# Kernel tuning notes

Measured on AMD Instinct MI355X. Metric: run time of the kernel, lower is better.

## Reference

```python
import jax, jax.numpy as jnp
import numpy as np

D_MODEL = 256
N_HEAD = 8


def setup_inputs() -> dict:
    key = jax.random.key(0)
    ks = jax.random.split(key, 9)
    B, S, D = 2, 2048, D_MODEL
    s = 1.0 / np.sqrt(D)
    return {
        "x": jax.random.normal(ks[0], (B, S, D), dtype=jnp.float32),
        "wq": jax.random.uniform(ks[1], (D, D), jnp.float32, -s, s),
        "bq": jax.random.uniform(ks[2], (D,), jnp.float32, -s, s),
        "wk": jax.random.uniform(ks[3], (D, D), jnp.float32, -s, s),
        "bk": jax.random.uniform(ks[4], (D,), jnp.float32, -s, s),
        "wv": jax.random.uniform(ks[5], (D, D), jnp.float32, -s, s),
        "bv": jax.random.uniform(ks[6], (D,), jnp.float32, -s, s),
        "wc": jax.random.uniform(ks[7], (D, D), jnp.float32, -s, s),
        "bc": jax.random.uniform(ks[8], (D,), jnp.float32, -s, s),
    }


def _split_heads(t):
    # [B, S, D] -> [B, H, S, D/H]
    B, S, D = t.shape
    return t.reshape(B, S, N_HEAD, D // N_HEAD).transpose(0, 2, 1, 3)


def reference(x, wq, bq, wk, bk, wv, bv, wc, bc):
    q = _split_heads(x @ wq.T + bq)
    k = _split_heads(x @ wk.T + bk)
    v = _split_heads(x @ wv.T + bv)
    d_head = q.shape[-1]
    # full [B, H, S, S] score matrix, as in the original (non-fused)
    score = jnp.einsum("bhqd,bhkd->bhqk", q, k) / jnp.sqrt(jnp.float32(d_head))
    attn = jax.nn.softmax(score, axis=-1)
    out = jnp.einsum("bhqk,bhkd->bhqd", attn, v)
    B, H, S, Dh = out.shape
    out = out.transpose(0, 2, 1, 3).reshape(B, S, H * Dh)
    out = out @ wc.T + bc
    attention = jnp.mean(attn, axis=1)  # [B, S, S]
    return (out, attention)
```

## Files before the change

kernel.cpp:

```cpp
#include <hip/hip_runtime.h>
#include <hip/hip_bf16.h>


#define B_   2
#define S_   2048
#define D_   256
#define H_   8
#define DH_  32
#define NROW (B_*S_)
#define KSPLIT 4
#define KKEYS (S_/KSPLIT)

typedef __attribute__((ext_vector_type(8))) short bf16x8;
typedef __attribute__((ext_vector_type(4))) float f32x4;

__device__ __forceinline__ f32x4 mfma_bf16(bf16x8 a, bf16x8 b, f32x4 c) {
    return __builtin_amdgcn_mfma_f32_16x16x32_bf16(a, b, c, 0, 0, 0);
}

__device__ __forceinline__ float fast_exp2(float x) {
    return __builtin_amdgcn_exp2f(x);
}

__device__ __forceinline__ unsigned short f2bf_bits(float v) {
    __hip_bfloat16 h = __float2bfloat16(v);
    return *reinterpret_cast<unsigned short*>(&h);
}

__device__ __forceinline__ size_t fragidx(int m, int k) {
    return (size_t)(m >> 4) * 4096 + (k >> 5) * 512 + ((k >> 3) & 3) * 128
           + (m & 15) * 8 + (k & 7);
}

__global__ void split_all(const float4* __restrict__ x,
                          const float4* __restrict__ wq, const float4* __restrict__ wk,
                          const float4* __restrict__ wv, const float4* __restrict__ wc,
                          ushort4* __restrict__ xh, ushort4* __restrict__ xl,
                          ushort4* __restrict__ wqh, ushort4* __restrict__ wql,
                          ushort4* __restrict__ wkh, ushort4* __restrict__ wkl,
                          ushort4* __restrict__ wvh, ushort4* __restrict__ wvl,
                          ushort4* __restrict__ wch, ushort4* __restrict__ wcl) {
    int i = blockIdx.x * 256 + threadIdx.x;
    const float4* src; ushort4 *ph, *pl; int off;
    if (i < 262144) { src = x; ph = xh; pl = xl; off = i; }
    else {
        int j = i - 262144;
        int rg = j >> 14; off = j & 16383;
        if (rg == 0)      { src = wq; ph = wqh; pl = wql; }
        else if (rg == 1) { src = wk; ph = wkh; pl = wkl; }
        else if (rg == 2) { src = wv; ph = wvh; pl = wvl; }
        else              { src = wc; ph = wch; pl = wcl; }
    }
    float4 v = src[off];
    float vv[4] = {v.x, v.y, v.z, v.w};
    ushort4 hb, lb;
    unsigned short* hp = (unsigned short*)&hb;
    unsigned short* lp = (unsigned short*)&lb;
    for (int c = 0; c < 4; c++) {
        __hip_bfloat16 h = __float2bfloat16(vv[c]);
        hp[c] = *reinterpret_cast<unsigned short*>(&h);
        lp[c] = f2bf_bits(vv[c] - __bfloat162float(h));
    }
    int m = off >> 6, k = (off & 63) * 4;
    size_t fi = fragidx(m, k);
    ph[fi >> 2] = hb;
    pl[fi >> 2] = lb;
}

__global__ __launch_bounds__(256) void qkv_gemm(
    const __hip_bfloat16* __restrict__ xh, const __hip_bfloat16* __restrict__ xl,
    const __hip_bfloat16* __restrict__ w0h, const __hip_bfloat16* __restrict__ w0l,
    const __hip_bfloat16* __restrict__ w1h, const __hip_bfloat16* __restrict__ w1l,
    const __hip_bfloat16* __restrict__ w2h, const __hip_bfloat16* __restrict__ w2l,
    const float* __restrict__ bq, const float* __restrict__ bk, const float* __restrict__ bvv,
    __hip_bfloat16* __restrict__ Qf, __hip_bfloat16* __restrict__ Kf,
    __hip_bfloat16* __restrict__ Vf)
{
    int z = blockIdx.z;
    const __hip_bfloat16* wh = (z==0) ? w0h : (z==1) ? w1h : w2h;
    const __hip_bfloat16* wl = (z==0) ? w0l : (z==1) ? w1l : w2l;
    const float* bias = (z==0) ? bq : (z==1) ? bk : bvv;
    const float sv = (z==0) ? 0.17677669529663687f * 1.4426950408889634f : 1.0f;

    int tid = threadIdx.x;
    int w = tid >> 6, lid = tid & 63, quad = lid >> 4, l15 = lid & 15;
    int row0 = blockIdx.x * 64 + (w >> 1) * 32;
    int col0 = blockIdx.y * 64 + (w & 1) * 32;

    f32x4 acc[2][2] = {};
#pragma unroll
    for (int k0 = 0; k0 < 256; k0 += 32) {
        bf16x8 ah[2], al[2], bh[2], bl[2];
        for (int mi = 0; mi < 2; mi++) {
            size_t ro = (size_t)((row0 + mi * 16) >> 4) * 4096 + (k0 >> 5) * 512 + lid * 8;
            ah[mi] = *(const bf16x8*)(xh + ro);
            al[mi] = *(const bf16x8*)(xl + ro);
        }
        for (int ni = 0; ni < 2; ni++) {
            size_t co = (size_t)((col0 + ni * 16) >> 4) * 4096 + (k0 >> 5) * 512 + lid * 8;
            bh[ni] = *(const bf16x8*)(wh + co);
            bl[ni] = *(const bf16x8*)(wl + co);
        }
        for (int mi = 0; mi < 2; mi++)
            for (int ni = 0; ni < 2; ni++) {
                acc[mi][ni] = mfma_bf16(ah[mi], bh[ni], acc[mi][ni]);
                acc[mi][ni] = mfma_bf16(ah[mi], bl[ni], acc[mi][ni]);
                acc[mi][ni] = mfma_bf16(al[mi], bh[ni], acc[mi][ni]);
            }
    }
    for (int mi = 0; mi < 2; mi++)
        for (int ni = 0; ni < 2; ni++) {
            int col = col0 + ni * 16 + l15;
            int h = col >> 5, dh = col & 31;
            float bvl = bias[col];
            for (int r = 0; r < 4; r++) {
                int row = row0 + mi * 16 + quad * 4 + r;
                int b = row >> 11, s = row & 2047;
                __hip_bfloat16 o = __float2bfloat16((acc[mi][ni][r] + bvl) * sv);
                size_t bh_base = (size_t)(b * H_ + h) * (S_ * DH_);
                if (z == 2) {
                    int oo = s & 31;
                    int slot = ((oo & 15) >> 2) * 8 + ((oo >> 4) << 2) + (oo & 3);
                    Vf[bh_base + (s >> 5) * 1024 + (dh >> 4) * 512
                       + (slot >> 3) * 128 + (dh & 15) * 8 + (slot & 7)] = o;
                } else {
                    size_t idx = bh_base + (s >> 4) * 512 + (dh >> 3) * 128
                                 + (s & 15) * 8 + (dh & 7);
                    if (z == 0) Qf[idx] = o; else Kf[idx] = o;
                }
            }
        }
}

__global__ __launch_bounds__(256) void attn_flash(
    const __hip_bfloat16* __restrict__ Qf, const __hip_bfloat16* __restrict__ Kf,
    const __hip_bfloat16* __restrict__ Vf,
    __hip_bfloat16* __restrict__ cth, __hip_bfloat16* __restrict__ ctl,
    float* __restrict__ invL)
{
    __shared__ float sO[KSPLIT][32][33];
    __shared__ float sL[KSPLIT][32];
    int f = blockIdx.x;
    int g = (f & 7) * 128 + (f >> 3);
    int qt = g & 63;
    int h = (g >> 6) & 7;
    int b = g >> 9;
    int q0 = qt * 32;
    int tid = threadIdx.x, w = tid >> 6, lid = tid & 63, quad = lid >> 4, l15 = lid & 15;
    size_t bh_base = (size_t)(b * H_ + h) * (S_ * DH_);
    const __hip_bfloat16* Qp = Qf + bh_base + (q0 >> 4) * 512 + lid * 8;
    const __hip_bfloat16* Kp = Kf + bh_base + lid * 8;
    const __hip_bfloat16* Vp = Vf + bh_base + lid * 8;
    bf16x8 qfA = *(const bf16x8*)Qp;
    bf16x8 qfB = *(const bf16x8*)(Qp + 512);
    f32x4 zacc = {};
    f32x4 oacc[2][2] = {};
    float lpA = 0.f, lpB = 0.f;

    int kbeg = w * KKEYS;
#pragma unroll 2
    for (int k0 = kbeg; k0 < kbeg + KKEYS; k0 += 32) {
        bf16x8 kf0 = *(const bf16x8*)(Kp + (k0 >> 4) * 512);
        bf16x8 kf1 = *(const bf16x8*)(Kp + (k0 >> 4) * 512 + 512);
        bf16x8 vf0 = *(const bf16x8*)(Vp + (k0 >> 5) * 1024);
        bf16x8 vf1 = *(const bf16x8*)(Vp + (k0 >> 5) * 1024 + 512);

        __builtin_amdgcn_s_setprio(1);
        f32x4 cA0 = mfma_bf16(kf0, qfA, zacc);
        f32x4 cA1 = mfma_bf16(kf1, qfA, zacc);
        f32x4 cB0 = mfma_bf16(kf0, qfB, zacc);
        f32x4 cB1 = mfma_bf16(kf1, qfB, zacc);
        __builtin_amdgcn_s_setprio(0);
        float eA0[4], eA1[4], eB0[4], eB1[4];
        for (int r = 0; r < 4; r++) {
            eA0[r] = fast_exp2(cA0[r]);
            eA1[r] = fast_exp2(cA1[r]);
            eB0[r] = fast_exp2(cB0[r]);
            eB1[r] = fast_exp2(cB1[r]);
        }
        lpA += eA0[0] + eA0[1] + eA0[2] + eA0[3] + eA1[0] + eA1[1] + eA1[2] + eA1[3];
        lpB += eB0[0] + eB0[1] + eB0[2] + eB0[3] + eB1[0] + eB1[1] + eB1[2] + eB1[3];
        union { bf16x8 v; __hip_bfloat162 h2[4]; } puA, puB;
        puA.h2[0] = __float22bfloat162_rn(make_float2(eA0[0], eA0[1]));
        puA.h2[1] = __float22bfloat162_rn(make_float2(eA0[2], eA0[3]));
        puA.h2[2] = __float22bfloat162_rn(make_float2(eA1[0], eA1[1]));
        puA.h2[3] = __float22bfloat162_rn(make_float2(eA1[2], eA1[3]));
        puB.h2[0] = __float22bfloat162_rn(make_float2(eB0[0], eB0[1]));
        puB.h2[1] = __float22bfloat162_rn(make_float2(eB0[2], eB0[3]));
        puB.h2[2] = __float22bfloat162_rn(make_float2(eB1[0], eB1[1]));
        puB.h2[3] = __float22bfloat162_rn(make_float2(eB1[2], eB1[3]));
        __builtin_amdgcn_s_setprio(1);
        oacc[0][0] = mfma_bf16(vf0, puA.v, oacc[0][0]);
        oacc[0][1] = mfma_bf16(vf1, puA.v, oacc[0][1]);
        oacc[1][0] = mfma_bf16(vf0, puB.v, oacc[1][0]);
        oacc[1][1] = mfma_bf16(vf1, puB.v, oacc[1][1]);
        __builtin_amdgcn_s_setprio(0);
    }
    lpA += __shfl_xor(lpA, 16);
    lpA += __shfl_xor(lpA, 32);
    lpB += __shfl_xor(lpB, 16);
    lpB += __shfl_xor(lpB, 32);

    for (int qg = 0; qg < 2; qg++)
        for (int dh2 = 0; dh2 < 2; dh2++)
            for (int r = 0; r < 4; r++)
                sO[w][qg * 16 + l15][dh2 * 16 + quad * 4 + r] = oacc[qg][dh2][r];
    if (lid < 16) { sL[w][lid] = lpA; sL[w][16 + lid] = lpB; }
    __syncthreads();

    int d = tid & 31, q = tid >> 5;
#pragma unroll
    for (int qq = q; qq < 32; qq += 8) {
        float l = sL[0][qq] + sL[1][qq] + sL[2][qq] + sL[3][qq];
        float o = sO[0][qq][d] + sO[1][qq][d] + sO[2][qq][d] + sO[3][qq][d];
        float inv = 1.0f / l;
        float val = o * inv;
        size_t fi = fragidx(b * S_ + q0 + qq, h * DH_ + d);
        __hip_bfloat16 hv = __float2bfloat16(val);
        cth[fi] = hv;
        ctl[fi] = __float2bfloat16(val - __bfloat162float(hv));
        if (d == 0) invL[(b * H_ + h) * S_ + q0 + qq] = inv;
    }
}

__global__ __launch_bounds__(256) void attn_out(
    const __hip_bfloat16* __restrict__ Qf, const __hip_bfloat16* __restrict__ Kf,
    const float* __restrict__ invL,
    const __hip_bfloat16* __restrict__ ch, const __hip_bfloat16* __restrict__ cl,
    const __hip_bfloat16* __restrict__ wh, const __hip_bfloat16* __restrict__ wl,
    const float* __restrict__ bias,
    float* __restrict__ attn, float* __restrict__ out)
{
    __shared__ float invbuf[H_ * 32];
    int bid = blockIdx.x;
    int tid = threadIdx.x, w = tid >> 6, lid = tid & 63, quad = lid >> 4, l15 = lid & 15;

    if (bid < 256) {
        int row0 = (bid & 63) * 64 + (w >> 1) * 32;
        int col0 = (bid >> 6) * 64 + (w & 1) * 32;

        f32x4 acc[2][2] = {};
#pragma unroll
        for (int k0 = 0; k0 < 256; k0 += 32) {
            bf16x8 ah[2], al[2], bh[2], bl[2];
            for (int mi = 0; mi < 2; mi++) {
                size_t ro = (size_t)((row0 + mi * 16) >> 4) * 4096 + (k0 >> 5) * 512 + lid * 8;
                ah[mi] = *(const bf16x8*)(ch + ro);
                al[mi] = *(const bf16x8*)(cl + ro);
            }
            for (int ni = 0; ni < 2; ni++) {
                size_t co = (size_t)((col0 + ni * 16) >> 4) * 4096 + (k0 >> 5) * 512 + lid * 8;
                bh[ni] = *(const bf16x8*)(wh + co);
                bl[ni] = *(const bf16x8*)(wl + co);
            }
            for (int mi = 0; mi < 2; mi++)
                for (int ni = 0; ni < 2; ni++) {
                    acc[mi][ni] = mfma_bf16(ah[mi], bh[ni], acc[mi][ni]);
                    acc[mi][ni] = mfma_bf16(ah[mi], bl[ni], acc[mi][ni]);
                    acc[mi][ni] = mfma_bf16(al[mi], bh[ni], acc[mi][ni]);
                }
        }
        for (int mi = 0; mi < 2; mi++)
            for (int ni = 0; ni < 2; ni++) {
                int col = col0 + ni * 16 + l15;
                float bvl = bias[col];
                for (int r = 0; r < 4; r++) {
                    int row = row0 + mi * 16 + quad * 4 + r;
                    out[(size_t)row * 256 + col] = acc[mi][ni][r] + bvl;
                }
            }
    } else {
        int f2 = bid - 256;
        int g = (f2 & 7) * 128 + (f2 >> 3);
        int qy = g & 63, kx = (g >> 6) & 7, b = g >> 9;
        int q0 = qy * 32;
        int k0 = kx * 256 + w * 64;
        invbuf[tid] = invL[(b * H_ + (tid >> 5)) * S_ + q0 + (tid & 31)] * 0.125f;
        __syncthreads();
        f32x4 zacc = {};
        float psum[2][4][4] = {};
        size_t bh0 = (size_t)b * H_ * (S_ * DH_);
        size_t qoff = (size_t)(q0 >> 4) * 512 + lid * 8;
        size_t koff = (size_t)(k0 >> 4) * 512 + lid * 8;

#pragma unroll 2
        for (int h = 0; h < H_; h++) {
            size_t nb = bh0 + (size_t)h * (S_ * DH_);
            bf16x8 qfA = *(const bf16x8*)(Qf + nb + qoff);
            bf16x8 qfB = *(const bf16x8*)(Qf + nb + qoff + 512);
            bf16x8 kf0 = *(const bf16x8*)(Kf + nb + koff);
            bf16x8 kf1 = *(const bf16x8*)(Kf + nb + koff + 512);
            bf16x8 kf2 = *(const bf16x8*)(Kf + nb + koff + 1024);
            bf16x8 kf3 = *(const bf16x8*)(Kf + nb + koff + 1536);

            float ilA[4], ilB[4];
            for (int r = 0; r < 4; r++) {
                ilA[r] = invbuf[h * 32 + quad * 4 + r];
                ilB[r] = invbuf[h * 32 + 16 + quad * 4 + r];
            }

            __builtin_amdgcn_s_setprio(1);
            f32x4 cA0 = mfma_bf16(qfA, kf0, zacc);
            f32x4 cA1 = mfma_bf16(qfA, kf1, zacc);
            f32x4 cA2 = mfma_bf16(qfA, kf2, zacc);
            f32x4 cA3 = mfma_bf16(qfA, kf3, zacc);
            f32x4 cB0 = mfma_bf16(qfB, kf0, zacc);
            f32x4 cB1 = mfma_bf16(qfB, kf1, zacc);
            f32x4 cB2 = mfma_bf16(qfB, kf2, zacc);
            f32x4 cB3 = mfma_bf16(qfB, kf3, zacc);
            __builtin_amdgcn_s_setprio(0);
            for (int r = 0; r < 4; r++) {
                psum[0][0][r] += fast_exp2(cA0[r]) * ilA[r];
                psum[0][1][r] += fast_exp2(cA1[r]) * ilA[r];
                psum[0][2][r] += fast_exp2(cA2[r]) * ilA[r];
                psum[0][3][r] += fast_exp2(cA3[r]) * ilA[r];
                psum[1][0][r] += fast_exp2(cB0[r]) * ilB[r];
                psum[1][1][r] += fast_exp2(cB1[r]) * ilB[r];
                psum[1][2][r] += fast_exp2(cB2[r]) * ilB[r];
                psum[1][3][r] += fast_exp2(cB3[r]) * ilB[r];
            }
        }
        for (int qg = 0; qg < 2; qg++)
            for (int nt = 0; nt < 4; nt++)
                for (int r = 0; r < 4; r++)
                    attn[(size_t)(b * S_ + q0 + qg * 16 + quad * 4 + r) * S_
                         + k0 + nt * 16 + l15] = psum[qg][nt][r];
    }
}

extern "C" void kernel_launch(void* const* d_in, const int* in_sizes, int n_in,
                              void* d_out, int out_size, void* d_ws, size_t ws_size,
                              hipStream_t stream) {
    const float* x  = (const float*)d_in[0];
    const float* wq = (const float*)d_in[1];
    const float* bq = (const float*)d_in[2];
    const float* wk = (const float*)d_in[3];
    const float* bk = (const float*)d_in[4];
    const float* wv = (const float*)d_in[5];
    const float* bv = (const float*)d_in[6];
    const float* wc = (const float*)d_in[7];
    const float* bc = (const float*)d_in[8];

    char* ws = (char*)d_ws;
    const size_t MB = 1u << 20;
    const size_t KB128 = 128u * 1024u;
    __hip_bfloat16* xh  = (__hip_bfloat16*)(ws + 0 * MB);
    __hip_bfloat16* xl  = (__hip_bfloat16*)(ws + 2 * MB);
    __hip_bfloat16* wqh = (__hip_bfloat16*)(ws + 4 * MB + 0 * KB128);
    __hip_bfloat16* wql = (__hip_bfloat16*)(ws + 4 * MB + 1 * KB128);
    __hip_bfloat16* wkh = (__hip_bfloat16*)(ws + 4 * MB + 2 * KB128);
    __hip_bfloat16* wkl = (__hip_bfloat16*)(ws + 4 * MB + 3 * KB128);
    __hip_bfloat16* wvh = (__hip_bfloat16*)(ws + 4 * MB + 4 * KB128);
    __hip_bfloat16* wvl = (__hip_bfloat16*)(ws + 4 * MB + 5 * KB128);
    __hip_bfloat16* wch = (__hip_bfloat16*)(ws + 4 * MB + 6 * KB128);
    __hip_bfloat16* wcl = (__hip_bfloat16*)(ws + 4 * MB + 7 * KB128);
    __hip_bfloat16* Qfb = (__hip_bfloat16*)(ws + 5 * MB);
    __hip_bfloat16* Kfb = (__hip_bfloat16*)(ws + 7 * MB);
    __hip_bfloat16* Vfb = (__hip_bfloat16*)(ws + 9 * MB);
    __hip_bfloat16* cth = (__hip_bfloat16*)(ws + 11 * MB);
    __hip_bfloat16* ctl = (__hip_bfloat16*)(ws + 13 * MB);
    float* invL  = (float*)(ws + 15 * MB);

    float* outp  = (float*)d_out;
    float* attnp = outp + (size_t)NROW * D_;

    hipLaunchKernelGGL(split_all, dim3(1280), dim3(256), 0, stream,
                       (const float4*)x, (const float4*)wq, (const float4*)wk,
                       (const float4*)wv, (const float4*)wc,
                       (ushort4*)xh, (ushort4*)xl,
                       (ushort4*)wqh, (ushort4*)wql, (ushort4*)wkh, (ushort4*)wkl,
                       (ushort4*)wvh, (ushort4*)wvl, (ushort4*)wch, (ushort4*)wcl);

    hipLaunchKernelGGL(qkv_gemm, dim3(NROW / 64, 4, 3), dim3(256), 0, stream,
                       xh, xl, wqh, wql, wkh, wkl, wvh, wvl, bq, bk, bv, Qfb, Kfb, Vfb);

    hipLaunchKernelGGL(attn_flash, dim3(1024), dim3(256), 0, stream,
                       Qfb, Kfb, Vfb, cth, ctl, invL);

    hipLaunchKernelGGL(attn_out, dim3(256 + 1024), dim3(256), 0, stream,
                       Qfb, Kfb, invL, cth, ctl, wch, wcl, bc, attnp, outp);
}
```

Baseline: 127.0 us.

## Double query tile to 64 rows in flash and attention-map kernels

The query tile per block in attn_flash and in the attention-mean part of attn_out grows from 32 to 64 rows, so each K/V fragment loaded is reused across four 16-row query groups instead of two. Grid sizes are halved to match, and the shared buffers for partial outputs, row sums and inverse normalisers are enlarged. The change cuts global K/V traffic per query but raises register pressure and halves the number of blocks, which lowers parallelism on a GPU with many CUs. The setprio hints and unroll pragmas are also dropped.

```diff
diff --git a/kernel.cpp b/kernel.cpp
--- a/kernel.cpp
+++ b/kernel.cpp
@@ -138,81 +138,72 @@
     __hip_bfloat16* __restrict__ cth, __hip_bfloat16* __restrict__ ctl,
     float* __restrict__ invL)
 {
-    __shared__ float sO[KSPLIT][32][33];
-    __shared__ float sL[KSPLIT][32];
+    __shared__ float sO[KSPLIT][64][33];
+    __shared__ float sL[KSPLIT][64];
     int f = blockIdx.x;
-    int g = (f & 7) * 128 + (f >> 3);
-    int qt = g & 63;
-    int h = (g >> 6) & 7;
-    int b = g >> 9;
-    int q0 = qt * 32;
+    int g = (f & 7) * 64 + (f >> 3);
+    int qt = g & 31;
+    int h = (g >> 5) & 7;
+    int b = g >> 8;
+    int q0 = qt * 64;
     int tid = threadIdx.x, w = tid >> 6, lid = tid & 63, quad = lid >> 4, l15 = lid & 15;
     size_t bh_base = (size_t)(b * H_ + h) * (S_ * DH_);
     const __hip_bfloat16* Qp = Qf + bh_base + (q0 >> 4) * 512 + lid * 8;
     const __hip_bfloat16* Kp = Kf + bh_base + lid * 8;
     const __hip_bfloat16* Vp = Vf + bh_base + lid * 8;
-    bf16x8 qfA = *(const bf16x8*)Qp;
-    bf16x8 qfB = *(const bf16x8*)(Qp + 512);
+    bf16x8 qf[4];
+#pragma unroll
+    for (int i = 0; i < 4; i++) qf[i] = *(const bf16x8*)(Qp + i * 512);
     f32x4 zacc = {};
-    f32x4 oacc[2][2] = {};
-    float lpA = 0.f, lpB = 0.f;
+    f32x4 oacc[4][2] = {};
+    float lp[4] = {};
 
     int kbeg = w * KKEYS;
-#pragma unroll 2
     for (int k0 = kbeg; k0 < kbeg + KKEYS; k0 += 32) {
         bf16x8 kf0 = *(const bf16x8*)(Kp + (k0 >> 4) * 512);
         bf16x8 kf1 = *(const bf16x8*)(Kp + (k0 >> 4) * 512 + 512);
         bf16x8 vf0 = *(const bf16x8*)(Vp + (k0 >> 5) * 1024);
         bf16x8 vf1 = *(const bf16x8*)(Vp + (k0 >> 5) * 1024 + 512);
-
-        __builtin_amdgcn_s_setprio(1);
-        f32x4 cA0 = mfma_bf16(kf0, qfA, zacc);
-        f32x4 cA1 = mfma_bf16(kf1, qfA, zacc);
-        f32x4 cB0 = mfma_bf16(kf0, qfB, zacc);
-        f32x4 cB1 = mfma_bf16(kf1, qfB, zacc);
-        __builtin_amdgcn_s_setprio(0);
-        float eA0[4], eA1[4], eB0[4], eB1[4];
-        for (int r = 0; r < 4; r++) {
-            eA0[r] = fast_exp2(cA0[r]);
-            eA1[r] = fast_exp2(cA1[r]);
-            eB0[r] = fast_exp2(cB0[r]);
-            eB1[r] = fast_exp2(cB1[r]);
-        }
-        lpA += eA0[0] + eA0[1] + eA0[2] + eA0[3] + eA1[0] + eA1[1] + eA1[2] + eA1[3];
-        lpB += eB0[0] + eB0[1] + eB0[2] + eB0[3] + eB1[0] + eB1[1] + eB1[2] + eB1[3];
-        union { bf16x8 v; __hip_bfloat162 h2[4]; } puA, puB;
-        puA.h2[0] = __float22bfloat162_rn(make_float2(eA0[0], eA0[1]));
-        puA.h2[1] = __float22bfloat162_rn(make_float2(eA0[2], eA0[3]));
-        puA.h2[2] = __float22bfloat162_rn(make_float2(eA1[0], eA1[1]));
-        puA.h2[3] = __float22bfloat162_rn(make_float2(eA1[2], eA1[3]));
-        puB.h2[0] = __float22bfloat162_rn(make_float2(eB0[0], eB0[1]));
-        puB.h2[1] = __float22bfloat162_rn(make_float2(eB0[2], eB0[3]));
-        puB.h2[2] = __float22bfloat162_rn(make_float2(eB1[0], eB1[1]));
-        puB.h2[3] = __float22bfloat162_rn(make_float2(eB1[2], eB1[3]));
-        __builtin_amdgcn_s_setprio(1);
-        oacc[0][0] = mfma_bf16(vf0, puA.v, oacc[0][0]);
-        oacc[0][1] = mfma_bf16(vf1, puA.v, oacc[0][1]);
-        oacc[1][0] = mfma_bf16(vf0, puB.v, oacc[1][0]);
-        oacc[1][1] = mfma_bf16(vf1, puB.v, oacc[1][1]);
-        __builtin_amdgcn_s_setprio(0);
-    }
-    lpA += __shfl_xor(lpA, 16);
-    lpA += __shfl_xor(lpA, 32);
-    lpB += __shfl_xor(lpB, 16);
-    lpB += __shfl_xor(lpB, 32);
-
-    for (int qg = 0; qg < 2; qg++)
+#pragma unroll
+        for (int qg = 0; qg < 4; qg++) {
+            f32x4 c0 = mfma_bf16(kf0, qf[qg], zacc);
+            f32x4 c1 = mfma_bf16(kf1, qf[qg], zacc);
+            float e0[4], e1[4];
+            for (int r = 0; r < 4; r++) {
+                e0[r] = fast_exp2(c0[r]);
+                e1[r] = fast_exp2(c1[r]);
+            }
+            lp[qg] += ((e0[0] + e0[1]) + (e0[2] + e0[3]))
+                    + ((e1[0] + e1[1]) + (e1[2] + e1[3]));
+            union { bf16x8 v; __hip_bfloat162 h2[4]; } pu;
+            pu.h2[0] = __float22bfloat162_rn(make_float2(e0[0], e0[1]));
+            pu.h2[1] = __float22bfloat162_rn(make_float2(e0[2], e0[3]));
+            pu.h2[2] = __float22bfloat162_rn(make_float2(e1[0], e1[1]));
+            pu.h2[3] = __float22bfloat162_rn(make_float2(e1[2], e1[3]));
+            oacc[qg][0] = mfma_bf16(vf0, pu.v, oacc[qg][0]);
+            oacc[qg][1] = mfma_bf16(vf1, pu.v, oacc[qg][1]);
+        }
+    }
+#pragma unroll
+    for (int qg = 0; qg < 4; qg++) {
+        lp[qg] += __shfl_xor(lp[qg], 16);
+        lp[qg] += __shfl_xor(lp[qg], 32);
+    }
+
+#pragma unroll
+    for (int qg = 0; qg < 4; qg++)
         for (int dh2 = 0; dh2 < 2; dh2++)
             for (int r = 0; r < 4; r++)
                 sO[w][qg * 16 + l15][dh2 * 16 + quad * 4 + r] = oacc[qg][dh2][r];
-    if (lid < 16) { sL[w][lid] = lpA; sL[w][16 + lid] = lpB; }
+    if (lid < 16)
+        for (int qg = 0; qg < 4; qg++) sL[w][qg * 16 + lid] = lp[qg];
     __syncthreads();
 
     int d = tid & 31, q = tid >> 5;
 #pragma unroll
-    for (int qq = q; qq < 32; qq += 8) {
-        float l = sL[0][qq] + sL[1][qq] + sL[2][qq] + sL[3][qq];
-        float o = sO[0][qq][d] + sO[1][qq][d] + sO[2][qq][d] + sO[3][qq][d];
+    for (int qq = q; qq < 64; qq += 8) {
+        float l = (sL[0][qq] + sL[1][qq]) + (sL[2][qq] + sL[3][qq]);
+        float o = (sO[0][qq][d] + sO[1][qq][d]) + (sO[2][qq][d] + sO[3][qq][d]);
         float inv = 1.0f / l;
         float val = o * inv;
         size_t fi = fragidx(b * S_ + q0 + qq, h * DH_ + d);
@@ -231,7 +222,7 @@
     const float* __restrict__ bias,
     float* __restrict__ attn, float* __restrict__ out)
 {
-    __shared__ float invbuf[H_ * 32];
+    __shared__ float invbuf[H_ * 64];
     int bid = blockIdx.x;
     int tid = threadIdx.x, w = tid >> 6, lid = tid & 63, quad = lid >> 4, l15 = lid & 15;
 
@@ -271,56 +262,46 @@
             }
     } else {
         int f2 = bid - 256;
-        int g = (f2 & 7) * 128 + (f2 >> 3);
-        int qy = g & 63, kx = (g >> 6) & 7, b = g >> 9;
-        int q0 = qy * 32;
+        int g = (f2 & 7) * 64 + (f2 >> 3);
+        int qy = g & 31, kx = (g >> 5) & 7, b = g >> 8;
+        int q0 = qy * 64;
         int k0 = kx * 256 + w * 64;
-        invbuf[tid] = invL[(b * H_ + (tid >> 5)) * S_ + q0 + (tid & 31)] * 0.125f;
+        invbuf[tid] = invL[(b * H_ + (tid >> 6)) * S_ + q0 + (tid & 63)] * 0.125f;
+        invbuf[tid + 256] =
+            invL[(b * H_ + 4 + (tid >> 6)) * S_ + q0 + (tid & 63)] * 0.125f;
         __syncthreads();
         f32x4 zacc = {};
-        float psum[2][4][4] = {};
+        float psum[4][4][4] = {};
         size_t bh0 = (size_t)b * H_ * (S_ * DH_);
         size_t qoff = (size_t)(q0 >> 4) * 512 + lid * 8;
         size_t koff = (size_t)(k0 >> 4) * 512 + lid * 8;
 
-#pragma unroll 2
         for (int h = 0; h < H_; h++) {
             size_t nb = bh0 + (size_t)h * (S_ * DH_);
-            bf16x8 qfA = *(const bf16x8*)(Qf + nb + qoff);
-            bf16x8 qfB = *(const bf16x8*)(Qf + nb + qoff + 512);
             bf16x8 kf0 = *(const bf16x8*)(Kf + nb + koff);
             bf16x8 kf1 = *(const bf16x8*)(Kf + nb + koff + 512);
             bf16x8 kf2 = *(const bf16x8*)(Kf + nb + koff + 1024);
             bf16x8 kf3 = *(const bf16x8*)(Kf + nb + koff + 1536);
-
-            float ilA[4], ilB[4];
-            for (int r = 0; r < 4; r++) {
-                ilA[r] = invbuf[h * 32 + quad * 4 + r];
-                ilB[r] = invbuf[h * 32 + 16 + quad * 4 + r];
-            }
-
-            __builtin_amdgcn_s_setprio(1);
-            f32x4 cA0 = mfma_bf16(qfA, kf0, zacc);
-            f32x4 cA1 = mfma_bf16(qfA, kf1, zacc);
-            f32x4 cA2 = mfma_bf16(qfA, kf2, zacc);
-            f32x4 cA3 = mfma_bf16(qfA, kf3, zacc);
-            f32x4 cB0 = mfma_bf16(qfB, kf0, zacc);
-            f32x4 cB1 = mfma_bf16(qfB, kf1, zacc);
-            f32x4 cB2 = mfma_bf16(qfB, kf2, zacc);
-            f32x4 cB3 = mfma_bf16(qfB, kf3, zacc);
-            __builtin_amdgcn_s_setprio(0);
-            for (int r = 0; r < 4; r++) {
-                psum[0][0][r] += fast_exp2(cA0[r]) * ilA[r];
-                psum[0][1][r] += fast_exp2(cA1[r]) * ilA[r];
-                psum[0][2][r] += fast_exp2(cA2[r]) * ilA[r];
-                psum[0][3][r] += fast_exp2(cA3[r]) * ilA[r];
-                psum[1][0][r] += fast_exp2(cB0[r]) * ilB[r];
-                psum[1][1][r] += fast_exp2(cB1[r]) * ilB[r];
-                psum[1][2][r] += fast_exp2(cB2[r]) * ilB[r];
-                psum[1][3][r] += fast_exp2(cB3[r]) * ilB[r];
-            }
-        }
-        for (int qg = 0; qg < 2; qg++)
+#pragma unroll
+            for (int qg = 0; qg < 4; qg++) {
+                bf16x8 qfg = *(const bf16x8*)(Qf + nb + qoff + qg * 512);
+                float il[4];
+                for (int r = 0; r < 4; r++)
+                    il[r] = invbuf[h * 64 + qg * 16 + quad * 4 + r];
+                f32x4 c0 = mfma_bf16(qfg, kf0, zacc);
+                f32x4 c1 = mfma_bf16(qfg, kf1, zacc);
+                f32x4 c2 = mfma_bf16(qfg, kf2, zacc);
+                f32x4 c3 = mfma_bf16(qfg, kf3, zacc);
+                for (int r = 0; r < 4; r++) {
+                    psum[qg][0][r] += fast_exp2(c0[r]) * il[r];
+                    psum[qg][1][r] += fast_exp2(c1[r]) * il[r];
+                    psum[qg][2][r] += fast_exp2(c2[r]) * il[r];
+                    psum[qg][3][r] += fast_exp2(c3[r]) * il[r];
+                }
+            }
+        }
+#pragma unroll
+        for (int qg = 0; qg < 4; qg++)
             for (int nt = 0; nt < 4; nt++)
                 for (int r = 0; r < 4; r++)
                     attn[(size_t)(b * S_ + q0 + qg * 16 + quad * 4 + r) * S_
@@ -374,9 +355,9 @@
     hipLaunchKernelGGL(qkv_gemm, dim3(NROW / 64, 4, 3), dim3(256), 0, stream,
                        xh, xl, wqh, wql, wkh, wkl, wvh, wvl, bq, bk, bv, Qfb, Kfb, Vfb);
 
-    hipLaunchKernelGGL(attn_flash, dim3(1024), dim3(256), 0, stream,
+    hipLaunchKernelGGL(attn_flash, dim3(512), dim3(256), 0, stream,
                        Qfb, Kfb, Vfb, cth, ctl, invL);
 
-    hipLaunchKernelGGL(attn_out, dim3(256 + 1024), dim3(256), 0, stream,
+    hipLaunchKernelGGL(attn_out, dim3(256 + 512), dim3(256), 0, stream,
                        Qfb, Kfb, invL, cth, ctl, wch, wcl, bc, attnp, outp);
 }
```

Result: slower. 135.3 us (+6.5%).
